# Kernel tuning notes

Measured on AMD Instinct MI355X. Metric: run time of the kernel, lower is better.

The kernel has to match this reference:

```python
import jax, jax.numpy as jnp
import numpy as np

B, S, D = 2, 2048, 1024
H = 16
HD = D // H  # 64


def setup_inputs() -> dict:
    key = jax.random.key(0)
    ks = jax.random.split(key, 6)
    std = 1.0 / np.sqrt(D)
    x = jax.random.normal(ks[0], (B, S, D), dtype=jnp.float32)
    Wq = jax.random.uniform(ks[1], (D, D), jnp.float32, -std, std)
    Wk = jax.random.uniform(ks[2], (D, D), jnp.float32, -std, std)
    Wv = jax.random.uniform(ks[3], (D, D), jnp.float32, -std, std)
    Wo = jax.random.uniform(ks[4], (D, D), jnp.float32, -std, std)
    bo = jax.random.uniform(ks[5], (D,), jnp.float32, -std, std)
    return {"x": x, "Wq": Wq, "Wk": Wk, "Wv": Wv, "Wo": Wo, "bo": bo}


def reference(x, Wq, Wk, Wv, Wo, bo):
    b, n, _ = x.shape
    # project and split heads: [b, H, n, HD]
    def split_heads(y):
        return y.reshape(b, n, H, HD).transpose(0, 2, 1, 3)
    q = split_heads(jnp.einsum('bnd,ed->bne', x, Wq))
    k = split_heads(jnp.einsum('bnd,ed->bne', x, Wk))
    v = split_heads(jnp.einsum('bnd,ed->bne', x, Wv))
    scores = jnp.einsum('bhqd,bhkd->bhqk', q, k)
    causal = jnp.triu(jnp.ones((n, n), dtype=bool), k=1)
    # original masks with -inf BEFORE scaling; -inf/scale == -inf so math matches
    scores = jnp.where(causal, -jnp.inf, scores) / jnp.sqrt(jnp.asarray(HD, scores.dtype))
    attn = jax.nn.softmax(scores, axis=-1)
    ctx = jnp.einsum('bhqk,bhkd->bhqd', attn, v)
    ctx = ctx.transpose(0, 2, 1, 3).reshape(b, n, D)
    return jnp.einsum('bnd,ed->bne', ctx, Wo) + bo
```

## Files before the change

kernel.cpp:

```cpp
#include <hip/hip_runtime.h>

#define DEV __device__ __forceinline__

typedef __bf16 bf16x8 __attribute__((ext_vector_type(8)));
typedef float f32x4 __attribute__((ext_vector_type(4)));
typedef float f32x16 __attribute__((ext_vector_type(16)));
typedef unsigned u32x4 __attribute__((ext_vector_type(4)));

constexpr int S_LEN = 2048;
constexpr int DMODEL = 1024;
constexpr int NHEAD = 16;
constexpr int HDIM = 64;
constexpr int BATCH = 2;
constexpr int MROWS = BATCH * S_LEN;
constexpr float QSCALE = 0.125f * 1.44269504088896f;

DEV short f2bf(float x) {
  unsigned u = __builtin_bit_cast(unsigned, x);
  unsigned r = u + 0x7fffu + ((u >> 16) & 1u);
  return (short)(r >> 16);
}

#define MFMA16(a, b, c) __builtin_amdgcn_mfma_f32_16x16x32_bf16((a), (b), (c), 0, 0, 0)
#define MFMA32(a, b, c) __builtin_amdgcn_mfma_f32_32x32x16_bf16((a), (b), (c), 0, 0, 0)
#define GLL16(g, l)                                                                     \
  __builtin_amdgcn_global_load_lds((const __attribute__((address_space(1))) void*)(g),  \
                                   (__attribute__((address_space(3))) void*)(l), 16, 0, 0)

DEV unsigned cvt_pk_bf16(float a, float b) {
  unsigned r;
  asm("v_cvt_pk_bf16_f32 %0, %1, %2" : "=v"(r) : "v"(a), "v"(b));
  return r;
}
DEV void swap32(unsigned& a, unsigned& b) {
  asm("v_permlane32_swap_b32 %0, %1" : "+v"(a), "+v"(b));
}

__global__ void cvt_kernel(const float* __restrict__ in, short* __restrict__ out, int n) {
  int i = (blockIdx.x * blockDim.x + threadIdx.x) * 4;
  const int stride = gridDim.x * blockDim.x * 4;
  for (; i < n; i += stride) {
    float4 v = *(const float4*)&in[i];
    short4 r;
    r.x = f2bf(v.x);
    r.y = f2bf(v.y);
    r.z = f2bf(v.z);
    r.w = f2bf(v.w);
    *(short4*)&out[i] = r;
  }
}

__global__ void cvt_w4(const float* __restrict__ Wq, const float* __restrict__ Wk,
                       const float* __restrict__ Wv, const float* __restrict__ Wo,
                       short* __restrict__ out) {
  const float* src = blockIdx.y == 0 ? Wq : blockIdx.y == 1 ? Wk : blockIdx.y == 2 ? Wv : Wo;
  short* dst = out + (size_t)blockIdx.y * (DMODEL * DMODEL);
  int i = (blockIdx.x * blockDim.x + threadIdx.x) * 4;
  const int stride = gridDim.x * blockDim.x * 4;
  for (; i < DMODEL * DMODEL; i += stride) {
    float4 v = *(const float4*)&src[i];
    short4 r;
    r.x = f2bf(v.x);
    r.y = f2bf(v.y);
    r.z = f2bf(v.z);
    r.w = f2bf(v.w);
    *(short4*)&dst[i] = r;
  }
}

__global__ __launch_bounds__(256) void gemm_bt(const short* __restrict__ A,
                                               const short* __restrict__ Bt,
                                               short* __restrict__ outb) {
  constexpr int K = DMODEL;
  constexpr size_t XN = (size_t)MROWS * DMODEL;
  __shared__ short As[2][128 * 64];
  __shared__ short Bs[2][128 * 64];
  const int tid = threadIdx.x;
  const int w = tid >> 6, l = tid & 63;
  const int lr = l & 15, lh = l >> 4;
  const int wr = w >> 1, wc = w & 1;
  const int tm = blockIdx.x, tn = blockIdx.y;
  const bool vswap = (tn >= 16);

  const int srow = tid >> 3;
  const int ssl = tid & 7;
  const int ssg = ssl ^ (srow & 7);

  f32x4 acc[4][4] = {};

#define GSTAGE(KT, BUF)                                                             \
  {                                                                                 \
    _Pragma("unroll") for (int i = 0; i < 4; ++i) {                                 \
      const int row = i * 32 + srow;                                                \
      GLL16(A + (size_t)(tm * 128 + row) * K + (KT)*64 + ssg * 8,                   \
            &As[BUF][(i * 256 + w * 64) * 8]);                                      \
    }                                                                               \
    _Pragma("unroll") for (int i = 0; i < 4; ++i) {                                 \
      const int row = i * 32 + srow;                                                \
      GLL16(Bt + (size_t)(tn * 128 + row) * K + (KT)*64 + ssg * 8,                  \
            &Bs[BUF][(i * 256 + w * 64) * 8]);                                      \
    }                                                                               \
  }

  GSTAGE(0, 0);
  asm volatile("s_waitcnt vmcnt(0)" ::: "memory");
  __syncthreads();

  for (int kt = 0; kt < K / 64; ++kt) {
    const int buf = kt & 1;
    if (kt < K / 64 - 1) GSTAGE(kt + 1, buf ^ 1);

#pragma unroll
    for (int kh = 0; kh < 2; ++kh) {
      bf16x8 af[4], bfr[4];
#pragma unroll
      for (int mi = 0; mi < 4; ++mi) {
        const int row = wr * 64 + mi * 16 + lr;
        af[mi] = *(const bf16x8*)&As[buf][row * 64 + 8 * ((kh * 4 + lh) ^ (row & 7))];
      }
#pragma unroll
      for (int ni = 0; ni < 4; ++ni) {
        const int row = wc * 64 + ni * 16 + lr;
        bfr[ni] = *(const bf16x8*)&Bs[buf][row * 64 + 8 * ((kh * 4 + lh) ^ (row & 7))];
      }
      if (vswap) {
#pragma unroll
        for (int mi = 0; mi < 4; ++mi)
#pragma unroll
          for (int ni = 0; ni < 4; ++ni)
            acc[mi][ni] = MFMA16(bfr[ni], af[mi], acc[mi][ni]);
      } else {
#pragma unroll
        for (int mi = 0; mi < 4; ++mi)
#pragma unroll
          for (int ni = 0; ni < 4; ++ni)
            acc[mi][ni] = MFMA16(af[mi], bfr[ni], acc[mi][ni]);
      }
    }

    asm volatile("s_waitcnt vmcnt(0)" ::: "memory");
    __syncthreads();
  }
#undef GSTAGE

  const int m0 = tm * 128 + wr * 64;
  const int n0 = tn * 128 + wc * 64;
  if (vswap) {
#pragma unroll
    for (int mi = 0; mi < 4; ++mi)
#pragma unroll
      for (int ni = 0; ni < 4; ++ni)
#pragma unroll
        for (int i = 0; i < 4; ++i) {
          const int e = n0 + ni * 16 + lh * 4 + i;
          const int m = m0 + mi * 16 + lr;
          const int ecol = e & (DMODEL - 1);
          const int b = m >> 11, n = m & (S_LEN - 1);
          const int h = ecol >> 6, d = ecol & (HDIM - 1);
          (outb + 2 * XN)[((size_t)((b * NHEAD + h) * HDIM + d)) * S_LEN + n] =
              f2bf(acc[mi][ni][i]);
        }
  } else {
    const int sel = tn >> 3;
#pragma unroll
    for (int mi = 0; mi < 4; ++mi)
#pragma unroll
      for (int ni = 0; ni < 4; ++ni)
#pragma unroll
        for (int i = 0; i < 4; ++i) {
          const int m = m0 + mi * 16 + lh * 4 + i;
          const int e = n0 + ni * 16 + lr;
          const int ecol = e & (DMODEL - 1);
          const int b = m >> 11, n = m & (S_LEN - 1);
          const int h = ecol >> 6, d = ecol & (HDIM - 1);
          if (sel == 0)
            outb[((size_t)((b * NHEAD + h) * S_LEN + n)) * HDIM + d] =
                f2bf(acc[mi][ni][i] * QSCALE);
          else
            (outb + XN)[((size_t)((b * NHEAD + h) * S_LEN + n)) * HDIM + d] =
                f2bf(acc[mi][ni][i]);
        }
  }
}

__global__ __launch_bounds__(256) void gemm_out(const short* __restrict__ A,
                                                const short* __restrict__ Bt,
                                                float* __restrict__ outf,
                                                const float* __restrict__ bias) {
  constexpr int K = DMODEL;
  constexpr int N = DMODEL;
  __shared__ short As[2][64 * 64];
  __shared__ short Bs[2][128 * 64];
  const int tid = threadIdx.x;
  const int w = tid >> 6, l = tid & 63;
  const int lr = l & 15, lh = l >> 4;
  const int wc = w;
  const int tm = blockIdx.x, tn = blockIdx.y;

  const int srow = tid >> 3;
  const int ssl = tid & 7;
  const int ssg = ssl ^ (srow & 7);

  f32x4 acc[4][2] = {};

#define OSTAGE(KT, BUF)                                                             \
  {                                                                                 \
    _Pragma("unroll") for (int i = 0; i < 2; ++i) {                                 \
      const int row = i * 32 + srow;                                                \
      GLL16(A + (size_t)(tm * 64 + row) * K + (KT)*64 + ssg * 8,                    \
            &As[BUF][(i * 256 + w * 64) * 8]);                                      \
    }                                                                               \
    _Pragma("unroll") for (int i = 0; i < 4; ++i) {                                 \
      const int row = i * 32 + srow;                                                \
      GLL16(Bt + (size_t)(tn * 128 + row) * K + (KT)*64 + ssg * 8,                  \
            &Bs[BUF][(i * 256 + w * 64) * 8]);                                      \
    }                                                                               \
  }

  OSTAGE(0, 0);
  asm volatile("s_waitcnt vmcnt(0)" ::: "memory");
  __syncthreads();

  for (int kt = 0; kt < K / 64; ++kt) {
    const int buf = kt & 1;
    if (kt < K / 64 - 1) OSTAGE(kt + 1, buf ^ 1);

#pragma unroll
    for (int kh = 0; kh < 2; ++kh) {
      bf16x8 af[4], bfr[2];
#pragma unroll
      for (int mi = 0; mi < 4; ++mi) {
        const int row = mi * 16 + lr;
        af[mi] = *(const bf16x8*)&As[buf][row * 64 + 8 * ((kh * 4 + lh) ^ (row & 7))];
      }
#pragma unroll
      for (int ni = 0; ni < 2; ++ni) {
        const int row = wc * 32 + ni * 16 + lr;
        bfr[ni] = *(const bf16x8*)&Bs[buf][row * 64 + 8 * ((kh * 4 + lh) ^ (row & 7))];
      }
#pragma unroll
      for (int mi = 0; mi < 4; ++mi)
#pragma unroll
        for (int ni = 0; ni < 2; ++ni)
          acc[mi][ni] = MFMA16(af[mi], bfr[ni], acc[mi][ni]);
    }

    asm volatile("s_waitcnt vmcnt(0)" ::: "memory");
    __syncthreads();
  }
#undef OSTAGE

#pragma unroll
  for (int mi = 0; mi < 4; ++mi)
#pragma unroll
    for (int ni = 0; ni < 2; ++ni)
#pragma unroll
      for (int i = 0; i < 4; ++i) {
        const int m = tm * 64 + mi * 16 + lh * 4 + i;
        const int e = tn * 128 + wc * 32 + ni * 16 + lr;
        outf[(size_t)m * N + e] = acc[mi][ni][i] + bias[e];
      }
}

__global__ __launch_bounds__(512) void attn_kernel(const short* __restrict__ Qg,
                                                   const short* __restrict__ Kg,
                                                   const short* __restrict__ Vg,
                                                   short* __restrict__ ctx) {
  __shared__ alignas(16) short KV[8][8192];
  __shared__ float mls[8][32];
  const int tidx = threadIdx.x;
  const int s = tidx >> 6;
  const int l = tidx & 63;
  const int lq = l & 31;
  const int h5 = l >> 5;
  const int bid = blockIdx.x;
  const int xcd = bid & 7;
  const int j = bid >> 3;
  const int bh = xcd * 4 + (j >> 6);
  const int qi = 63 - (j & 63);
  const int qbase = qi * 32;
  const short* Qh = Qg + (size_t)bh * (S_LEN * HDIM);
  const short* Kh = Kg + (size_t)bh * (S_LEN * HDIM);
  const short* Vh = Vg + (size_t)bh * (HDIM * S_LEN);

  short* Kbase = &KV[s][0];
  short* Vbase = &KV[s][4096];
  const int r8 = l >> 3;
  const int sc = l & 7;

  bf16x8 qf[4];
#pragma unroll
  for (int cc = 0; cc < 4; ++cc)
    qf[cc] = *(const bf16x8*)&Qh[(size_t)(qbase + lq) * HDIM + cc * 16 + h5 * 8];

  f32x16 o0 = {}, o1 = {};
  float ll = 0.f;

  const int ntot = qi + 1;
  const int ts = (ntot * s) >> 3;
  const int te = (ntot * (s + 1)) >> 3;

#define STAGE(T, BUF)                                                              \
  {                                                                                \
    _Pragma("unroll") for (int i = 0; i < 4; ++i) {                                \
      const int R = i * 8 + r8;                                                    \
      const int sg = sc ^ (R & 7);                                                 \
      GLL16(Kh + (size_t)((T)*32 + R) * HDIM + sg * 8,                             \
            &Kbase[(BUF)*2048 + i * 512]);                                         \
      GLL16(Vh + (size_t)(2 * R + (sg >> 2)) * S_LEN + (T)*32 + (sg & 3) * 8,      \
            &Vbase[(BUF)*2048 + i * 512]);                                         \
    }                                                                              \
  }

  if (ts < te) STAGE(ts, 0);

  for (int t = ts; t < te; ++t) {
    const int buf = (t - ts) & 1;
    if (t + 1 < te) {
      STAGE(t + 1, buf ^ 1);
      asm volatile("s_waitcnt vmcnt(8)" ::: "memory");
    } else {
      asm volatile("s_waitcnt vmcnt(0)" ::: "memory");
    }
    const short* Ksb = &Kbase[buf * 2048];
    const short* Vsb = &Vbase[buf * 2048];

    bf16x8 kf[4];
#pragma unroll
    for (int cc = 0; cc < 4; ++cc)
      kf[cc] = *(const bf16x8*)&Ksb[lq * 64 + 8 * ((cc * 2 + h5) ^ (lq & 7))];
    f32x16 st = {};
    __builtin_amdgcn_s_setprio(1);
#pragma unroll
    for (int cc = 0; cc < 4; ++cc) st = MFMA32(kf[cc], qf[cc], st);
    __builtin_amdgcn_s_setprio(0);

    if (t == qi) {
#pragma unroll
      for (int rr = 0; rr < 16; ++rr) {
        const int crow = (rr & 3) + 8 * (rr >> 2) + 4 * h5;
        if (crow > lq) st[rr] = -__builtin_inff();
      }
    }

#pragma unroll
    for (int rr = 0; rr < 16; ++rr) {
      st[rr] = __builtin_amdgcn_exp2f(st[rr]);
      ll += st[rr];
    }

    unsigned a0 = cvt_pk_bf16(st[0], st[1]), b0 = cvt_pk_bf16(st[4], st[5]);
    unsigned a1 = cvt_pk_bf16(st[2], st[3]), b1 = cvt_pk_bf16(st[6], st[7]);
    unsigned a2 = cvt_pk_bf16(st[8], st[9]), b2 = cvt_pk_bf16(st[12], st[13]);
    unsigned a3 = cvt_pk_bf16(st[10], st[11]), b3 = cvt_pk_bf16(st[14], st[15]);
    swap32(a0, b0);
    swap32(a1, b1);
    swap32(a2, b2);
    swap32(a3, b3);
    const u32x4 pw0 = {a0, a1, b0, b1};
    const u32x4 pw1 = {a2, a3, b2, b3};
    const bf16x8 pa0 = __builtin_bit_cast(bf16x8, pw0);
    const bf16x8 pa1 = __builtin_bit_cast(bf16x8, pw1);

    const int R0 = lq >> 1, p0 = (lq & 1) * 4 + h5;
    const int R1 = 16 + (lq >> 1);
    const bf16x8 v00 = *(const bf16x8*)&Vsb[R0 * 64 + 8 * ((p0 + 0) ^ (R0 & 7))];
    const bf16x8 v01 = *(const bf16x8*)&Vsb[R0 * 64 + 8 * ((p0 + 2) ^ (R0 & 7))];
    const bf16x8 v10 = *(const bf16x8*)&Vsb[R1 * 64 + 8 * ((p0 + 0) ^ (R1 & 7))];
    const bf16x8 v11 = *(const bf16x8*)&Vsb[R1 * 64 + 8 * ((p0 + 2) ^ (R1 & 7))];
    __builtin_amdgcn_s_setprio(1);
    o0 = MFMA32(pa0, v00, o0);
    o1 = MFMA32(pa0, v10, o1);
    o0 = MFMA32(pa1, v01, o0);
    o1 = MFMA32(pa1, v11, o1);
    __builtin_amdgcn_s_setprio(0);
  }
#undef STAGE

  float* me = (float*)&KV[s][0];
#pragma unroll
  for (int rr = 0; rr < 16; ++rr) {
    const int crow = (rr & 3) + 8 * (rr >> 2) + 4 * h5;
    me[crow * 64 + lq] = o0[rr];
    me[crow * 64 + 32 + lq] = o1[rr];
  }
  ll += __shfl_xor(ll, 32);
  if (h5 == 0) mls[s][lq] = ll;
  __syncthreads();

  const float* om = (const float*)&KV[0][0];
  const int b = bh >> 4, h = bh & (NHEAD - 1);
  const int r2 = tidx >> 4;
  const int d0 = (tidx & 15) * 4;
  float lsum = 0.f;
#pragma unroll
  for (int ss = 0; ss < 8; ++ss) lsum += mls[ss][r2];
  const float inv = __builtin_amdgcn_rcpf(lsum);
  const size_t base = (size_t)(b * S_LEN + qbase + r2) * DMODEL + h * HDIM + d0;
#pragma unroll
  for (int i = 0; i < 4; ++i) {
    const int o = r2 * 64 + d0 + i;
    float v = 0.f;
#pragma unroll
    for (int ss = 0; ss < 8; ++ss) v += om[ss * 4096 + o];
    ctx[base + i] = f2bf(v * inv);
  }
}

extern "C" void kernel_launch(void* const* d_in, const int* in_sizes, int n_in,
                              void* d_out, int out_size, void* d_ws, size_t ws_size,
                              hipStream_t stream) {
  const float* x = (const float*)d_in[0];
  const float* Wq = (const float*)d_in[1];
  const float* Wk = (const float*)d_in[2];
  const float* Wv = (const float*)d_in[3];
  const float* Wo = (const float*)d_in[4];
  const float* bo = (const float*)d_in[5];

  const size_t XN = (size_t)MROWS * DMODEL;
  const size_t WN = (size_t)DMODEL * DMODEL;

  short* ws = (short*)d_ws;
  short* xb = ws;
  short* Wqb = xb + XN;
  short* Wob = Wqb + 3 * WN;
  short* Qb = Wob + WN;
  short* Kb = Qb + XN;
  short* Vb = Kb + XN;
  short* ctxb = Vb + XN;
  if (ws_size < (5 * XN + 4 * WN) * sizeof(short)) return;

  cvt_kernel<<<2048, 256, 0, stream>>>(x, xb, (int)XN);
  cvt_w4<<<dim3(256, 4), 256, 0, stream>>>(Wq, Wk, Wv, Wo, Wqb);

  gemm_bt<<<dim3(MROWS / 128, 3 * DMODEL / 128), 256, 0, stream>>>(xb, Wqb, Qb);

  attn_kernel<<<2048, 512, 0, stream>>>(Qb, Kb, Vb, ctxb);

  gemm_out<<<dim3(MROWS / 64, DMODEL / 128), 256, 0, stream>>>(ctxb, Wob, (float*)d_out,
                                                               bo);
}
```

Baseline: 125.7 us.

## Process two 32-row query tiles per attention block to reuse K/V loads

The attention kernel now handles 64 query rows per block as two 32-row sub-tiles, with 4 waves splitting the KV range instead of 8 waves over 32 rows. Each staged K/V tile in shared memory feeds both query sub-tiles, halving K/V global traffic and staging per query row. The final cross-wave reduction shrinks from 8 to 4 partial sums. In exchange, each wave holds more accumulator registers and there are half as many blocks, so occupancy and load balance across the causal triangle may suffer.

```diff
diff --git a/kernel.cpp b/kernel.cpp
--- a/kernel.cpp
+++ b/kernel.cpp
@@ -262,12 +262,12 @@
       }
 }
 
-__global__ __launch_bounds__(512) void attn_kernel(const short* __restrict__ Qg,
+__global__ __launch_bounds__(256) void attn_kernel(const short* __restrict__ Qg,
                                                    const short* __restrict__ Kg,
                                                    const short* __restrict__ Vg,
                                                    short* __restrict__ ctx) {
-  __shared__ alignas(16) short KV[8][8192];
-  __shared__ float mls[8][32];
+  __shared__ alignas(16) short KV[4][8192];
+  __shared__ float mls[4][2][32];
   const int tidx = threadIdx.x;
   const int s = tidx >> 6;
   const int l = tidx & 63;
@@ -276,9 +276,9 @@
   const int bid = blockIdx.x;
   const int xcd = bid & 7;
   const int j = bid >> 3;
-  const int bh = xcd * 4 + (j >> 6);
-  const int qi = 63 - (j & 63);
-  const int qbase = qi * 32;
+  const int bh = xcd * 4 + (j >> 5);
+  const int qc = 31 - (j & 31);
+  const int qbase = qc * 64;
   const short* Qh = Qg + (size_t)bh * (S_LEN * HDIM);
   const short* Kh = Kg + (size_t)bh * (S_LEN * HDIM);
   const short* Vh = Vg + (size_t)bh * (HDIM * S_LEN);
@@ -288,17 +288,20 @@
   const int r8 = l >> 3;
   const int sc = l & 7;
 
-  bf16x8 qf[4];
-#pragma unroll
-  for (int cc = 0; cc < 4; ++cc)
-    qf[cc] = *(const bf16x8*)&Qh[(size_t)(qbase + lq) * HDIM + cc * 16 + h5 * 8];
-
-  f32x16 o0 = {}, o1 = {};
-  float ll = 0.f;
-
-  const int ntot = qi + 1;
-  const int ts = (ntot * s) >> 3;
-  const int te = (ntot * (s + 1)) >> 3;
+  bf16x8 qf0[4], qf1[4];
+#pragma unroll
+  for (int cc = 0; cc < 4; ++cc) {
+    qf0[cc] = *(const bf16x8*)&Qh[(size_t)(qbase + lq) * HDIM + cc * 16 + h5 * 8];
+    qf1[cc] = *(const bf16x8*)&Qh[(size_t)(qbase + 32 + lq) * HDIM + cc * 16 + h5 * 8];
+  }
+
+  f32x16 o00 = {}, o01 = {}, o10 = {}, o11 = {};
+  float ll0 = 0.f, ll1 = 0.f;
+
+  const int ntot = 2 * qc + 2;
+  const int td0 = 2 * qc, td1 = 2 * qc + 1;
+  const int ts = (ntot * s) >> 2;
+  const int te = (ntot * (s + 1)) >> 2;
 
 #define STAGE(T, BUF)                                                              \
   {                                                                                \
@@ -329,51 +332,88 @@
 #pragma unroll
     for (int cc = 0; cc < 4; ++cc)
       kf[cc] = *(const bf16x8*)&Ksb[lq * 64 + 8 * ((cc * 2 + h5) ^ (lq & 7))];
-    f32x16 st = {};
-    __builtin_amdgcn_s_setprio(1);
-#pragma unroll
-    for (int cc = 0; cc < 4; ++cc) st = MFMA32(kf[cc], qf[cc], st);
-    __builtin_amdgcn_s_setprio(0);
-
-    if (t == qi) {
-#pragma unroll
-      for (int rr = 0; rr < 16; ++rr) {
-        const int crow = (rr & 3) + 8 * (rr >> 2) + 4 * h5;
-        if (crow > lq) st[rr] = -__builtin_inff();
-      }
-    }
-
-#pragma unroll
-    for (int rr = 0; rr < 16; ++rr) {
-      st[rr] = __builtin_amdgcn_exp2f(st[rr]);
-      ll += st[rr];
-    }
-
-    unsigned a0 = cvt_pk_bf16(st[0], st[1]), b0 = cvt_pk_bf16(st[4], st[5]);
-    unsigned a1 = cvt_pk_bf16(st[2], st[3]), b1 = cvt_pk_bf16(st[6], st[7]);
-    unsigned a2 = cvt_pk_bf16(st[8], st[9]), b2 = cvt_pk_bf16(st[12], st[13]);
-    unsigned a3 = cvt_pk_bf16(st[10], st[11]), b3 = cvt_pk_bf16(st[14], st[15]);
-    swap32(a0, b0);
-    swap32(a1, b1);
-    swap32(a2, b2);
-    swap32(a3, b3);
-    const u32x4 pw0 = {a0, a1, b0, b1};
-    const u32x4 pw1 = {a2, a3, b2, b3};
-    const bf16x8 pa0 = __builtin_bit_cast(bf16x8, pw0);
-    const bf16x8 pa1 = __builtin_bit_cast(bf16x8, pw1);
-
     const int R0 = lq >> 1, p0 = (lq & 1) * 4 + h5;
     const int R1 = 16 + (lq >> 1);
     const bf16x8 v00 = *(const bf16x8*)&Vsb[R0 * 64 + 8 * ((p0 + 0) ^ (R0 & 7))];
     const bf16x8 v01 = *(const bf16x8*)&Vsb[R0 * 64 + 8 * ((p0 + 2) ^ (R0 & 7))];
     const bf16x8 v10 = *(const bf16x8*)&Vsb[R1 * 64 + 8 * ((p0 + 0) ^ (R1 & 7))];
     const bf16x8 v11 = *(const bf16x8*)&Vsb[R1 * 64 + 8 * ((p0 + 2) ^ (R1 & 7))];
-    __builtin_amdgcn_s_setprio(1);
-    o0 = MFMA32(pa0, v00, o0);
-    o1 = MFMA32(pa0, v10, o1);
-    o0 = MFMA32(pa1, v01, o0);
-    o1 = MFMA32(pa1, v11, o1);
-    __builtin_amdgcn_s_setprio(0);
+
+    if (t != td1) {
+      f32x16 st = {};
+      __builtin_amdgcn_s_setprio(1);
+#pragma unroll
+      for (int cc = 0; cc < 4; ++cc) st = MFMA32(kf[cc], qf0[cc], st);
+      __builtin_amdgcn_s_setprio(0);
+      if (t == td0) {
+#pragma unroll
+        for (int rr = 0; rr < 16; ++rr) {
+          const int crow = (rr & 3) + 8 * (rr >> 2) + 4 * h5;
+          if (crow > lq) st[rr] = -__builtin_inff();
+        }
+      }
+#pragma unroll
+      for (int rr = 0; rr < 16; ++rr) {
+        st[rr] = __builtin_amdgcn_exp2f(st[rr]);
+        ll0 += st[rr];
+      }
+      unsigned a0 = cvt_pk_bf16(st[0], st[1]), b0 = cvt_pk_bf16(st[4], st[5]);
+      unsigned a1 = cvt_pk_bf16(st[2], st[3]), b1 = cvt_pk_bf16(st[6], st[7]);
+      unsigned a2 = cvt_pk_bf16(st[8], st[9]), b2 = cvt_pk_bf16(st[12], st[13]);
+      unsigned a3 = cvt_pk_bf16(st[10], st[11]), b3 = cvt_pk_bf16(st[14], st[15]);
+      swap32(a0, b0);
+      swap32(a1, b1);
+      swap32(a2, b2);
+      swap32(a3, b3);
+      const u32x4 pw0 = {a0, a1, b0, b1};
+      const u32x4 pw1 = {a2, a3, b2, b3};
+      const bf16x8 pa0 = __builtin_bit_cast(bf16x8, pw0);
+      const bf16x8 pa1 = __builtin_bit_cast(bf16x8, pw1);
+      __builtin_amdgcn_s_setprio(1);
+      o00 = MFMA32(pa0, v00, o00);
+      o01 = MFMA32(pa0, v10, o01);
+      o00 = MFMA32(pa1, v01, o00);
+      o01 = MFMA32(pa1, v11, o01);
+      __builtin_amdgcn_s_setprio(0);
+    }
+
+    {
+      f32x16 st = {};
+      __builtin_amdgcn_s_setprio(1);
+#pragma unroll
+      for (int cc = 0; cc < 4; ++cc) st = MFMA32(kf[cc], qf1[cc], st);
+      __builtin_amdgcn_s_setprio(0);
+      if (t == td1) {
+#pragma unroll
+        for (int rr = 0; rr < 16; ++rr) {
+          const int crow = (rr & 3) + 8 * (rr >> 2) + 4 * h5;
+          if (crow > lq) st[rr] = -__builtin_inff();
+        }
+      }
+#pragma unroll
+      for (int rr = 0; rr < 16; ++rr) {
+        st[rr] = __builtin_amdgcn_exp2f(st[rr]);
+        ll1 += st[rr];
+      }
+      unsigned a0 = cvt_pk_bf16(st[0], st[1]), b0 = cvt_pk_bf16(st[4], st[5]);
+      unsigned a1 = cvt_pk_bf16(st[2], st[3]), b1 = cvt_pk_bf16(st[6], st[7]);
+      unsigned a2 = cvt_pk_bf16(st[8], st[9]), b2 = cvt_pk_bf16(st[12], st[13]);
+      unsigned a3 = cvt_pk_bf16(st[10], st[11]), b3 = cvt_pk_bf16(st[14], st[15]);
+      swap32(a0, b0);
+      swap32(a1, b1);
+      swap32(a2, b2);
+      swap32(a3, b3);
+      const u32x4 pw0 = {a0, a1, b0, b1};
+      const u32x4 pw1 = {a2, a3, b2, b3};
+      const bf16x8 pa0 = __builtin_bit_cast(bf16x8, pw0);
+      const bf16x8 pa1 = __builtin_bit_cast(bf16x8, pw1);
+      __builtin_amdgcn_s_setprio(1);
+      o10 = MFMA32(pa0, v00, o10);
+      o11 = MFMA32(pa0, v10, o11);
+      o10 = MFMA32(pa1, v01, o10);
+      o11 = MFMA32(pa1, v11, o11);
+      __builtin_amdgcn_s_setprio(0);
+    }
   }
 #undef STAGE
 
@@ -381,28 +421,31 @@
 #pragma unroll
   for (int rr = 0; rr < 16; ++rr) {
     const int crow = (rr & 3) + 8 * (rr >> 2) + 4 * h5;
-    me[crow * 64 + lq] = o0[rr];
-    me[crow * 64 + 32 + lq] = o1[rr];
-  }
-  ll += __shfl_xor(ll, 32);
-  if (h5 == 0) mls[s][lq] = ll;
+    me[crow * 64 + lq] = o00[rr];
+    me[crow * 64 + 32 + lq] = o01[rr];
+    me[(32 + crow) * 64 + lq] = o10[rr];
+    me[(32 + crow) * 64 + 32 + lq] = o11[rr];
+  }
+  ll0 += __shfl_xor(ll0, 32);
+  ll1 += __shfl_xor(ll1, 32);
+  if (h5 == 0) {
+    mls[s][0][lq] = ll0;
+    mls[s][1][lq] = ll1;
+  }
   __syncthreads();
 
   const float* om = (const float*)&KV[0][0];
   const int b = bh >> 4, h = bh & (NHEAD - 1);
-  const int r2 = tidx >> 4;
-  const int d0 = (tidx & 15) * 4;
-  float lsum = 0.f;
-#pragma unroll
-  for (int ss = 0; ss < 8; ++ss) lsum += mls[ss][r2];
+  const int r2 = tidx >> 2;
+  const int d0 = (tidx & 3) * 16;
+  const float lsum = mls[0][r2 >> 5][r2 & 31] + mls[1][r2 >> 5][r2 & 31] +
+                     mls[2][r2 >> 5][r2 & 31] + mls[3][r2 >> 5][r2 & 31];
   const float inv = __builtin_amdgcn_rcpf(lsum);
   const size_t base = (size_t)(b * S_LEN + qbase + r2) * DMODEL + h * HDIM + d0;
 #pragma unroll
-  for (int i = 0; i < 4; ++i) {
+  for (int i = 0; i < 16; ++i) {
     const int o = r2 * 64 + d0 + i;
-    float v = 0.f;
-#pragma unroll
-    for (int ss = 0; ss < 8; ++ss) v += om[ss * 4096 + o];
+    const float v = om[o] + om[4096 + o] + om[8192 + o] + om[12288 + o];
     ctx[base + i] = f2bf(v * inv);
   }
 }
@@ -435,7 +478,7 @@
 
   gemm_bt<<<dim3(MROWS / 128, 3 * DMODEL / 128), 256, 0, stream>>>(xb, Wqb, Qb);
 
-  attn_kernel<<<2048, 512, 0, stream>>>(Qb, Kb, Vb, ctxb);
+  attn_kernel<<<1024, 256, 0, stream>>>(Qb, Kb, Vb, ctxb);
 
   gemm_out<<<dim3(MROWS / 64, DMODEL / 128), 256, 0, stream>>>(ctxb, Wob, (float*)d_out,
                                                                bo);
```

Result: faster. 118.4 us (-5.8%).
